# Kernel optimization log

Hardware: AMD Instinct MI355X
Metric: run time of the kernel (lower is better)

Reference implementation:

```python
import jax, jax.numpy as jnp
import numpy as np
import math

T = 4096          # num tokens (== context_window_len)
IN_SIZE = 2048    # model dim
HEAD_SIZE = 128   # per-head dim


def setup_inputs() -> dict:
    key = jax.random.key(0)
    kx, kq, kk, kv = jax.random.split(key, 4)
    scale = 1.0 / math.sqrt(IN_SIZE)
    x = jax.random.normal(kx, (T, IN_SIZE), dtype=jnp.float32)
    # eqx.nn.Linear(in, out) weight has shape [out, in], applied as W @ x
    Wq = jax.random.normal(kq, (HEAD_SIZE, IN_SIZE), dtype=jnp.float32) * scale
    Wk = jax.random.normal(kk, (HEAD_SIZE, IN_SIZE), dtype=jnp.float32) * scale
    Wv = jax.random.normal(kv, (HEAD_SIZE, IN_SIZE), dtype=jnp.float32) * scale
    return {"x": x, "Wq": Wq, "Wk": Wk, "Wv": Wv}


def reference(x, Wq, Wk, Wv):
    # q, k, v: [T, head_size]
    q = x @ Wq.T
    k = x @ Wk.T
    v = x @ Wv.T
    # scores: [T, T]
    scores = (q @ k.T) / math.sqrt(HEAD_SIZE)
    num_toks = x.shape[0]
    # causal mask: True above the diagonal (masked out)
    causal_mask = ~jnp.tril(jnp.ones((num_toks, num_toks), dtype=bool))
    masked = jnp.where(causal_mask, -jnp.inf, scores)
    attn = jax.nn.softmax(masked, axis=-1)
    return attn @ v
```

## Files before the change

### kernel.cpp

```cpp
#include <hip/hip_runtime.h>
#include <hip/hip_bf16.h>

#define T_TOK 4096
#define D_IN  2048
#define HS    128
#define CKV   4
#define NCH   16

typedef unsigned short u16;
typedef __attribute__((ext_vector_type(8))) __bf16 bf16x8;
typedef __attribute__((ext_vector_type(4))) float f32x4;
typedef __attribute__((ext_vector_type(4))) unsigned short us4;
typedef __attribute__((ext_vector_type(8))) unsigned short us8;

#define GLOBAL_AS __attribute__((address_space(1)))
#define LDS_AS    __attribute__((address_space(3)))

__device__ __forceinline__ void async_ld16(const void* g, void* l) {
  __builtin_amdgcn_global_load_lds((GLOBAL_AS void*)(void*)g, (LDS_AS void*)l, 16, 0, 0);
}

__device__ __forceinline__ u16 f2bf(float v) {
  return __builtin_bit_cast(u16, __float2bfloat16(v));
}

__device__ __forceinline__ bool detect_f32(const u16* in, int tid, int* sflag) {
  if (tid < 64) {
    int cnt = 0;
#pragma unroll
    for (int j = 0; j < 8; j++) {
      u16 v = in[(tid * 8 + j) * 2];
      cnt += (((v >> 7) & 0xFF) >= 0xBF) ? 1 : 0;
    }
#pragma unroll
    for (int off = 1; off < 64; off <<= 1) cnt += __shfl_xor(cnt, off);
    if (tid == 0) *sflag = (cnt > 8) ? 1 : 0;
  }
  __syncthreads();
  return (*sflag != 0);
}

__global__ __launch_bounds__(256) void cvt_kernel(
    const u16* __restrict__ w0, const u16* __restrict__ w1,
    const u16* __restrict__ w2, const u16* __restrict__ x,
    u16* __restrict__ o0, u16* __restrict__ o1, u16* __restrict__ o2,
    u16* __restrict__ xb, int* __restrict__ flag) {
  __shared__ int sflag;
  const int b = blockIdx.x;
  const int tid = threadIdx.x;
  if (b < 384) {
    const int mat = b >> 7;
    const int blk = b & 127;
    const u16* in = (mat == 0) ? w0 : ((mat == 1) ? w1 : w2);
    u16* out = (mat == 0) ? o0 : ((mat == 1) ? o1 : o2);
    const bool isf32 = detect_f32(in, tid, &sflag);
    if (tid == 0 && b == 0) *flag = isf32 ? 1 : 0;
    const size_t base = ((size_t)blk * 256 + tid) * 8;
    if (isf32) {
      const float* f = (const float*)in;
      us4 a, c;
#pragma unroll
      for (int j = 0; j < 4; j++) a[j] = f2bf(f[base + j]);
#pragma unroll
      for (int j = 0; j < 4; j++) c[j] = f2bf(f[base + 4 + j]);
      *(us4*)(out + base) = a;
      *(us4*)(out + base + 4) = c;
    } else {
      *(us8*)(out + base) = *(const us8*)(in + base);
    }
  } else {
    const bool isf32 = detect_f32(x, tid, &sflag);
    if (!isf32) return;
    const int blk = b - 384;
    const size_t base = ((size_t)blk * 256 + tid) * 8;
    const float* f = (const float*)x;
    us4 a, c;
#pragma unroll
    for (int j = 0; j < 4; j++) a[j] = f2bf(f[base + j]);
#pragma unroll
    for (int j = 0; j < 4; j++) c[j] = f2bf(f[base + 4 + j]);
    *(us4*)(xb + base) = a;
    *(us4*)(xb + base + 4) = c;
  }
}

__global__ __launch_bounds__(256, 2) void qkv_kernel(
    const u16* __restrict__ x, const u16* __restrict__ xb,
    const u16* __restrict__ Wq, const u16* __restrict__ Wk,
    const u16* __restrict__ Wv,
    u16* __restrict__ Q, u16* __restrict__ K, u16* __restrict__ Vt)
{
  __shared__ __align__(16) u16 As[3][32 * 64];
  __shared__ __align__(16) u16 Bs[3][128 * 64];
  __shared__ int sflag;

  const int mat = blockIdx.y;
  const u16* W = (mat == 0) ? Wq : ((mat == 1) ? Wk : Wv);
  const int row0 = blockIdx.x * 32;
  const int tid = threadIdx.x;
  const int wv = tid >> 6, lane = tid & 63, l15 = lane & 15, quad = lane >> 4;

  const bool isf32 = detect_f32(x, tid, &sflag);
  const u16* A = isf32 ? xb : x;

  f32x4 acc[2][2];
#pragma unroll
  for (int i = 0; i < 2; i++)
#pragma unroll
    for (int j = 0; j < 2; j++) acc[i][j] = (f32x4)0.0f;

  auto stage = [&](int k0, int buf) {
    {
      int id = wv * 64 + lane;
      int r = id >> 3, c = (id & 7) ^ (r & 7);
      async_ld16(A + (size_t)(row0 + r) * D_IN + k0 + c * 8,
                 (char*)As[buf] + (size_t)wv * 1024);
    }
#pragma unroll
    for (int j = 0; j < 4; j++) {
      int id = j * 256 + wv * 64 + lane;
      int n = id >> 3, c = (id & 7) ^ (n & 7);
      async_ld16(W + (size_t)n * D_IN + k0 + c * 8,
                 (char*)Bs[buf] + (size_t)j * 4096 + (size_t)wv * 1024);
    }
  };

  stage(0, 0);
  stage(64, 1);

  for (int kt = 0; kt < 32; kt++) {
    const int cur = kt % 3;
    if (kt < 31) {
      asm volatile("s_waitcnt vmcnt(5) lgkmcnt(0)" ::: "memory");
    } else {
      asm volatile("s_waitcnt vmcnt(0) lgkmcnt(0)" ::: "memory");
    }
    __builtin_amdgcn_s_barrier();
    __builtin_amdgcn_sched_barrier(0);
    if (kt + 2 < 32) stage((kt + 2) * 64, (kt + 2) % 3);

    __builtin_amdgcn_s_setprio(1);
#pragma unroll
    for (int kc = 0; kc < 2; kc++) {
      const int cl = kc * 4 + quad;
#pragma unroll
      for (int mi = 0; mi < 2; mi++) {
        const int rA = mi * 16 + l15;
        bf16x8 a = *(const bf16x8*)((const char*)As[cur] + (rA * 8 + (cl ^ (rA & 7))) * 16);
#pragma unroll
        for (int nt = 0; nt < 2; nt++) {
          const int n = wv * 32 + nt * 16 + l15;
          bf16x8 b = *(const bf16x8*)((const char*)Bs[cur] + (n * 8 + (cl ^ (n & 7))) * 16);
          acc[mi][nt] = __builtin_amdgcn_mfma_f32_16x16x32_bf16(a, b, acc[mi][nt], 0, 0, 0);
        }
      }
    }
    __builtin_amdgcn_s_setprio(0);
  }

  if (mat < 2) {
    u16* out = (mat == 0) ? Q : K;
#pragma unroll
    for (int mi = 0; mi < 2; mi++)
#pragma unroll
      for (int nt = 0; nt < 2; nt++)
#pragma unroll
        for (int r = 0; r < 4; r++) {
          int m = row0 + mi * 16 + quad * 4 + r;
          int n = wv * 32 + nt * 16 + l15;
          out[(size_t)m * HS + n] = f2bf(acc[mi][nt][r]);
        }
  } else {
#pragma unroll
    for (int mi = 0; mi < 2; mi++)
#pragma unroll
      for (int nt = 0; nt < 2; nt++) {
        int n = wv * 32 + nt * 16 + l15;
        int mb = row0 + mi * 16 + quad * 4;
        us4 pk;
#pragma unroll
        for (int r = 0; r < 4; r++) pk[r] = f2bf(acc[mi][nt][r]);
        *(us4*)(Vt + (size_t)n * T_TOK + mb) = pk;
      }
  }
}

__global__ __launch_bounds__(256, 2) void attn_split_kernel(
    const u16* __restrict__ Q, const u16* __restrict__ Kg,
    const u16* __restrict__ Vt, float* __restrict__ Opart,
    float* __restrict__ mstat, float* __restrict__ lstat)
{
  __shared__ __align__(16) u16 Ks[2][64 * 128];
  __shared__ __align__(16) u16 Vs[2][128 * 64];
  __shared__ __align__(16) u16 Ps[4 * 16 * 64];

  const int qtile = 63 - (int)blockIdx.x;
  const int ch = blockIdx.y;
  if (4 * ch > qtile) return;
  const int t0 = 4 * ch;
  const int nsteps = min(CKV, qtile + 1 - t0);
  const int q0 = qtile * 64;
  const int slot = 64 * ch - 2 * ch * (ch - 1) + (qtile - 4 * ch);

  const int tid = threadIdx.x;
  const int wv = tid >> 6, lane = tid & 63, l15 = lane & 15, quad = lane >> 4;

  bf16x8 qf[4];
#pragma unroll
  for (int kc = 0; kc < 4; kc++)
    qf[kc] = *(const bf16x8*)(Q + (size_t)(q0 + 16 * wv + l15) * HS + kc * 32 + quad * 8);

  f32x4 o[8];
#pragma unroll
  for (int i = 0; i < 8; i++) o[i] = (f32x4)0.0f;
  float mrun[4], lrun[4];
#pragma unroll
  for (int r = 0; r < 4; r++) { mrun[r] = -1e30f; lrun[r] = 0.0f; }

  const float sc = 0.12752761571239668f;

  auto stage = [&](int t, int buf) {
#pragma unroll
    for (int j = 0; j < 4; j++) {
      int s = (wv * 4 + j) * 64 + lane;
      int n = s >> 4, cs = s & 15, c = cs ^ (n & 7);
      async_ld16(Kg + (size_t)(t * 64 + n) * HS + c * 8,
                 (char*)Ks[buf] + (size_t)(wv * 4 + j) * 1024);
    }
#pragma unroll
    for (int j = 0; j < 4; j++) {
      int s = (wv * 4 + j) * 64 + lane;
      int vr = s >> 3, cs = s & 7, c = cs ^ (vr & 7);
      async_ld16(Vt + (size_t)vr * T_TOK + t * 64 + c * 8,
                 (char*)Vs[buf] + (size_t)(wv * 4 + j) * 1024);
    }
  };

  stage(t0, 0);
  for (int i = 0; i < nsteps; i++) {
    const int cur = i & 1;
    const int t = t0 + i;
    __syncthreads();
    if (i + 1 < nsteps) stage(t + 1, 1 - cur);

    f32x4 sacc[4];
#pragma unroll
    for (int nt = 0; nt < 4; nt++) sacc[nt] = (f32x4)0.0f;
    __builtin_amdgcn_s_setprio(1);
#pragma unroll
    for (int kc = 0; kc < 4; kc++) {
      const int cl = kc * 4 + quad;
#pragma unroll
      for (int nt = 0; nt < 4; nt++) {
        int n = 16 * nt + l15;
        bf16x8 b = *(const bf16x8*)((const char*)Ks[cur] + (n * 16 + (cl ^ (n & 7))) * 16);
        sacc[nt] = __builtin_amdgcn_mfma_f32_16x16x32_bf16(qf[kc], b, sacc[nt], 0, 0, 0);
      }
    }
    __builtin_amdgcn_s_setprio(0);

    float s2[4][4];
    const bool diag = (t == qtile);
#pragma unroll
    for (int nt = 0; nt < 4; nt++)
#pragma unroll
      for (int r = 0; r < 4; r++) {
        float v = sacc[nt][r] * sc;
        if (diag) {
          int qr = q0 + 16 * wv + quad * 4 + r;
          int kr = t * 64 + 16 * nt + l15;
          if (kr > qr) v = -1e30f;
        }
        s2[nt][r] = v;
      }

    float mnew[4], alpha[4];
#pragma unroll
    for (int r = 0; r < 4; r++) {
      float tmax = fmaxf(fmaxf(s2[0][r], s2[1][r]), fmaxf(s2[2][r], s2[3][r]));
#pragma unroll
      for (int off = 1; off < 16; off <<= 1) tmax = fmaxf(tmax, __shfl_xor(tmax, off));
      mnew[r] = fmaxf(mrun[r], tmax);
      alpha[r] = exp2f(mrun[r] - mnew[r]);
      mrun[r] = mnew[r];
    }
    float p[4][4];
#pragma unroll
    for (int r = 0; r < 4; r++) {
      float s = 0.0f;
#pragma unroll
      for (int nt = 0; nt < 4; nt++) { p[nt][r] = exp2f(s2[nt][r] - mnew[r]); s += p[nt][r]; }
#pragma unroll
      for (int off = 1; off < 16; off <<= 1) s += __shfl_xor(s, off);
      lrun[r] = lrun[r] * alpha[r] + s;
    }
#pragma unroll
    for (int c = 0; c < 8; c++)
#pragma unroll
      for (int r = 0; r < 4; r++) o[c][r] *= alpha[r];

    u16* Pw = Ps + wv * 1024;
#pragma unroll
    for (int nt = 0; nt < 4; nt++)
#pragma unroll
      for (int r = 0; r < 4; r++) {
        int row = quad * 4 + r;
        int col = nt * 16 + l15;
        int cc = col >> 3, wi = col & 7;
        Pw[(row * 8 + (cc ^ (row & 7))) * 8 + wi] = f2bf(p[nt][r]);
      }

    __builtin_amdgcn_s_setprio(1);
#pragma unroll
    for (int kc = 0; kc < 2; kc++) {
      const int cl = kc * 4 + quad;
      bf16x8 a = *(const bf16x8*)((const char*)Pw + (l15 * 8 + (cl ^ (l15 & 7))) * 16);
#pragma unroll
      for (int c = 0; c < 8; c++) {
        int vr = 16 * c + l15;
        bf16x8 b = *(const bf16x8*)((const char*)Vs[cur] + (vr * 8 + (cl ^ (vr & 7))) * 16);
        o[c] = __builtin_amdgcn_mfma_f32_16x16x32_bf16(a, b, o[c], 0, 0, 0);
      }
    }
    __builtin_amdgcn_s_setprio(0);
  }

  float* po = Opart + (size_t)slot * 64 * 128;
#pragma unroll
  for (int c = 0; c < 8; c++)
#pragma unroll
    for (int r = 0; r < 4; r++) {
      int ml = 16 * wv + quad * 4 + r;
      po[ml * 128 + 16 * c + l15] = o[c][r];
    }
  if (l15 == 0) {
#pragma unroll
    for (int r = 0; r < 4; r++) {
      int ml = 16 * wv + quad * 4 + r;
      mstat[slot * 64 + ml] = mrun[r];
      lstat[slot * 64 + ml] = lrun[r];
    }
  }
}

__global__ __launch_bounds__(256) void combine_kernel(
    const float* __restrict__ Opart, const float* __restrict__ mstat,
    const float* __restrict__ lstat, void* __restrict__ out_v,
    const int* __restrict__ dflag)
{
  const int q = blockIdx.x;
  const int cb = blockIdx.y;
  const int tid = threadIdx.x;
  const int row = tid >> 2;
  const int col = cb * 32 + (tid & 3) * 8;
  const int nch = (q + 4) / 4;
  const bool of32 = (*dflag != 0);

  float M = -1e30f;
  {
    int base = 0;
    for (int c = 0; c < nch; c++) {
      int s = base + q - 4 * c;
      M = fmaxf(M, mstat[s * 64 + row]);
      base += 64 - 4 * c;
    }
  }
  float l = 0.0f;
  float acc[8];
#pragma unroll
  for (int j = 0; j < 8; j++) acc[j] = 0.0f;
  {
    int base = 0;
    for (int c = 0; c < nch; c++) {
      int s = base + q - 4 * c;
      float w = exp2f(mstat[s * 64 + row] - M);
      l += w * lstat[s * 64 + row];
      const float* op = Opart + ((size_t)s * 64 + row) * 128 + col;
      f32x4 a = *(const f32x4*)op;
      f32x4 b = *(const f32x4*)(op + 4);
#pragma unroll
      for (int j = 0; j < 4; j++) { acc[j] += w * a[j]; acc[4 + j] += w * b[j]; }
      base += 64 - 4 * c;
    }
  }
  const float inv = 1.0f / l;
  const size_t goff = (size_t)(q * 64 + row) * HS + col;
  if (of32) {
    float* out = (float*)out_v + goff;
    f32x4 r0, r1;
#pragma unroll
    for (int j = 0; j < 4; j++) { r0[j] = acc[j] * inv; r1[j] = acc[4 + j] * inv; }
    *(f32x4*)out = r0;
    *(f32x4*)(out + 4) = r1;
  } else {
    u16* out = (u16*)out_v + goff;
    us4 r0, r1;
#pragma unroll
    for (int j = 0; j < 4; j++) { r0[j] = f2bf(acc[j] * inv); r1[j] = f2bf(acc[4 + j] * inv); }
    *(us4*)out = r0;
    *(us4*)(out + 4) = r1;
  }
}

extern "C" void kernel_launch(void* const* d_in, const int* in_sizes, int n_in,
                              void* d_out, int out_size, void* d_ws, size_t ws_size,
                              hipStream_t stream) {
  const u16* x  = (const u16*)d_in[0];
  const u16* Wq = (const u16*)d_in[1];
  const u16* Wk = (const u16*)d_in[2];
  const u16* Wv = (const u16*)d_in[3];

  float* Opart = (float*)d_ws;
  float* mstat = Opart + (size_t)544 * 64 * 128;
  float* lstat = mstat + (size_t)544 * 64;

  u16* Wqb = (u16*)(lstat + (size_t)544 * 64);
  u16* Wkb = Wqb + (size_t)HS * D_IN;
  u16* Wvb = Wkb + (size_t)HS * D_IN;
  u16* Q   = Wvb + (size_t)HS * D_IN;
  u16* K   = Q   + (size_t)T_TOK * HS;
  u16* Vt  = K   + (size_t)T_TOK * HS;
  int* flag = (int*)(Vt + (size_t)T_TOK * HS);
  u16* xb  = (u16*)((char*)flag + 16);

  cvt_kernel<<<4480, 256, 0, stream>>>(Wq, Wk, Wv, x, Wqb, Wkb, Wvb, xb, flag);
  qkv_kernel<<<dim3(128, 3), 256, 0, stream>>>(x, xb, Wqb, Wkb, Wvb, Q, K, Vt);
  attn_split_kernel<<<dim3(64, NCH), 256, 0, stream>>>(Q, K, Vt, Opart, mstat, lstat);
  combine_kernel<<<dim3(64, 4), 256, 0, stream>>>(Opart, mstat, lstat, d_out, flag);
}
```

Measured before the change: 143.9 us.

## Fuse fp32-to-bf16 conversion of x into the QKV GEMM load path

Drops the separate pass that converts x from fp32 to bf16 into a workspace buffer. The QKV kernel now loads fp32 x tiles into registers, converts them, and writes bf16 into LDS, prefetching one step ahead, while the weight tiles keep the async LDS loads. This removes a full write and re-read of the 4096x2048 converted activation and shrinks the convert launch to the weights only. In exchange, the A-tile load is now synchronous through registers instead of async-to-LDS, and x is read three times in fp32 (once per Q/K/V matrix), which could stall the GEMM pipeline.

After: 141.0 us. 2.0% less time.

```diff
diff --git a/kernel.cpp b/kernel.cpp
--- a/kernel.cpp
+++ b/kernel.cpp
@@ -40,54 +40,36 @@
   return (*sflag != 0);
 }
 
-__global__ __launch_bounds__(256) void cvt_kernel(
+__global__ __launch_bounds__(256) void conv3_kernel(
     const u16* __restrict__ w0, const u16* __restrict__ w1,
-    const u16* __restrict__ w2, const u16* __restrict__ x,
-    u16* __restrict__ o0, u16* __restrict__ o1, u16* __restrict__ o2,
-    u16* __restrict__ xb, int* __restrict__ flag) {
+    const u16* __restrict__ w2, u16* __restrict__ o0,
+    u16* __restrict__ o1, u16* __restrict__ o2, int* __restrict__ flag) {
   __shared__ int sflag;
-  const int b = blockIdx.x;
+  const int mat = blockIdx.x >> 7;
+  const int blk = blockIdx.x & 127;
+  const u16* in = (mat == 0) ? w0 : ((mat == 1) ? w1 : w2);
+  u16* out = (mat == 0) ? o0 : ((mat == 1) ? o1 : o2);
   const int tid = threadIdx.x;
-  if (b < 384) {
-    const int mat = b >> 7;
-    const int blk = b & 127;
-    const u16* in = (mat == 0) ? w0 : ((mat == 1) ? w1 : w2);
-    u16* out = (mat == 0) ? o0 : ((mat == 1) ? o1 : o2);
-    const bool isf32 = detect_f32(in, tid, &sflag);
-    if (tid == 0 && b == 0) *flag = isf32 ? 1 : 0;
-    const size_t base = ((size_t)blk * 256 + tid) * 8;
-    if (isf32) {
-      const float* f = (const float*)in;
-      us4 a, c;
-#pragma unroll
-      for (int j = 0; j < 4; j++) a[j] = f2bf(f[base + j]);
-#pragma unroll
-      for (int j = 0; j < 4; j++) c[j] = f2bf(f[base + 4 + j]);
-      *(us4*)(out + base) = a;
-      *(us4*)(out + base + 4) = c;
-    } else {
-      *(us8*)(out + base) = *(const us8*)(in + base);
-    }
+  const bool isf32 = detect_f32(in, tid, &sflag);
+  if (tid == 0 && mat == 0 && blk == 0) *flag = isf32 ? 1 : 0;
+  const size_t base = ((size_t)blk * 256 + tid) * 8;
+  if (isf32) {
+    const float* f = (const float*)in;
+    us4 a, b;
+#pragma unroll
+    for (int j = 0; j < 4; j++) a[j] = f2bf(f[base + j]);
+#pragma unroll
+    for (int j = 0; j < 4; j++) b[j] = f2bf(f[base + 4 + j]);
+    *(us4*)(out + base) = a;
+    *(us4*)(out + base + 4) = b;
   } else {
-    const bool isf32 = detect_f32(x, tid, &sflag);
-    if (!isf32) return;
-    const int blk = b - 384;
-    const size_t base = ((size_t)blk * 256 + tid) * 8;
-    const float* f = (const float*)x;
-    us4 a, c;
-#pragma unroll
-    for (int j = 0; j < 4; j++) a[j] = f2bf(f[base + j]);
-#pragma unroll
-    for (int j = 0; j < 4; j++) c[j] = f2bf(f[base + 4 + j]);
-    *(us4*)(xb + base) = a;
-    *(us4*)(xb + base + 4) = c;
+    *(us8*)(out + base) = *(const us8*)(in + base);
   }
 }
 
 __global__ __launch_bounds__(256, 2) void qkv_kernel(
-    const u16* __restrict__ x, const u16* __restrict__ xb,
-    const u16* __restrict__ Wq, const u16* __restrict__ Wk,
-    const u16* __restrict__ Wv,
+    const u16* __restrict__ x, const u16* __restrict__ Wq,
+    const u16* __restrict__ Wk, const u16* __restrict__ Wv,
     u16* __restrict__ Q, u16* __restrict__ K, u16* __restrict__ Vt)
 {
   __shared__ __align__(16) u16 As[3][32 * 64];
@@ -101,7 +83,6 @@
   const int wv = tid >> 6, lane = tid & 63, l15 = lane & 15, quad = lane >> 4;
 
   const bool isf32 = detect_f32(x, tid, &sflag);
-  const u16* A = isf32 ? xb : x;
 
   f32x4 acc[2][2];
 #pragma unroll
@@ -109,13 +90,7 @@
 #pragma unroll
     for (int j = 0; j < 2; j++) acc[i][j] = (f32x4)0.0f;
 
-  auto stage = [&](int k0, int buf) {
-    {
-      int id = wv * 64 + lane;
-      int r = id >> 3, c = (id & 7) ^ (r & 7);
-      async_ld16(A + (size_t)(row0 + r) * D_IN + k0 + c * 8,
-                 (char*)As[buf] + (size_t)wv * 1024);
-    }
+  auto stageB = [&](int k0, int buf) {
 #pragma unroll
     for (int j = 0; j < 4; j++) {
       int id = j * 256 + wv * 64 + lane;
@@ -125,20 +100,7 @@
     }
   };
 
-  stage(0, 0);
-  stage(64, 1);
-
-  for (int kt = 0; kt < 32; kt++) {
-    const int cur = kt % 3;
-    if (kt < 31) {
-      asm volatile("s_waitcnt vmcnt(5) lgkmcnt(0)" ::: "memory");
-    } else {
-      asm volatile("s_waitcnt vmcnt(0) lgkmcnt(0)" ::: "memory");
-    }
-    __builtin_amdgcn_s_barrier();
-    __builtin_amdgcn_sched_barrier(0);
-    if (kt + 2 < 32) stage((kt + 2) * 64, (kt + 2) % 3);
-
+  auto compute = [&](int cur) {
     __builtin_amdgcn_s_setprio(1);
 #pragma unroll
     for (int kc = 0; kc < 2; kc++) {
@@ -156,6 +118,63 @@
       }
     }
     __builtin_amdgcn_s_setprio(0);
+  };
+
+  if (isf32) {
+    const int ar = tid >> 3;
+    const int ac = (tid & 7) ^ (ar & 7);
+    const float* ap = (const float*)x + (size_t)(row0 + ar) * D_IN + ac * 8;
+    f32x4 pa0, pa1;
+    auto loadA = [&](int k0) {
+      pa0 = *(const f32x4*)(ap + k0);
+      pa1 = *(const f32x4*)(ap + k0 + 4);
+    };
+    auto writeA = [&](int buf) {
+      us8 c0;
+#pragma unroll
+      for (int j = 0; j < 4; j++) { c0[j] = f2bf(pa0[j]); c0[4 + j] = f2bf(pa1[j]); }
+      *(us8*)((char*)As[buf] + (size_t)tid * 16) = c0;
+    };
+
+    stageB(0, 0);
+    loadA(0);
+    stageB(64, 1);
+
+    for (int kt = 0; kt < 32; kt++) {
+      const int cur = kt % 3;
+      writeA(cur);
+      asm volatile("s_waitcnt lgkmcnt(0)" ::: "memory");
+      __builtin_amdgcn_s_barrier();
+      __builtin_amdgcn_sched_barrier(0);
+      if (kt + 1 < 32) loadA((kt + 1) * 64);
+      if (kt + 2 < 32) stageB((kt + 2) * 64, (kt + 2) % 3);
+      compute(cur);
+    }
+  } else {
+    auto stageA = [&](int k0, int buf) {
+      int id = wv * 64 + lane;
+      int r = id >> 3, c = (id & 7) ^ (r & 7);
+      async_ld16(x + (size_t)(row0 + r) * D_IN + k0 + c * 8,
+                 (char*)As[buf] + (size_t)wv * 1024);
+    };
+    stageA(0, 0); stageB(0, 0);
+    stageA(64, 1); stageB(64, 1);
+
+    for (int kt = 0; kt < 32; kt++) {
+      const int cur = kt % 3;
+      if (kt < 31) {
+        asm volatile("s_waitcnt vmcnt(5) lgkmcnt(0)" ::: "memory");
+      } else {
+        asm volatile("s_waitcnt vmcnt(0) lgkmcnt(0)" ::: "memory");
+      }
+      __builtin_amdgcn_s_barrier();
+      __builtin_amdgcn_sched_barrier(0);
+      if (kt + 2 < 32) {
+        stageA((kt + 2) * 64, (kt + 2) % 3);
+        stageB((kt + 2) * 64, (kt + 2) % 3);
+      }
+      compute(cur);
+    }
   }
 
   if (mat < 2) {
@@ -421,10 +440,9 @@
   u16* K   = Q   + (size_t)T_TOK * HS;
   u16* Vt  = K   + (size_t)T_TOK * HS;
   int* flag = (int*)(Vt + (size_t)T_TOK * HS);
-  u16* xb  = (u16*)((char*)flag + 16);
-
-  cvt_kernel<<<4480, 256, 0, stream>>>(Wq, Wk, Wv, x, Wqb, Wkb, Wvb, xb, flag);
-  qkv_kernel<<<dim3(128, 3), 256, 0, stream>>>(x, xb, Wqb, Wkb, Wvb, Q, K, Vt);
+
+  conv3_kernel<<<384, 256, 0, stream>>>(Wq, Wk, Wv, Wqb, Wkb, Wvb, flag);
+  qkv_kernel<<<dim3(128, 3), 256, 0, stream>>>(x, Wqb, Wkb, Wvb, Q, K, Vt);
   attn_split_kernel<<<dim3(64, NCH), 256, 0, stream>>>(Q, K, Vt, Opart, mstat, lstat);
   combine_kernel<<<dim3(64, 4), 256, 0, stream>>>(Opart, mstat, lstat, d_out, flag);
 }
```
